# Performance work log

Hardware: AMD Instinct MI355X
Metric: run time of the kernel (lower is better)

Reference implementation:

```python
import jax, jax.numpy as jnp
import numpy as np

D_MODEL = 1024
N_EXPERTS = 8
TOP_K = 2
D_HIDDEN = 4 * D_MODEL


def setup_inputs() -> dict:
    key = jax.random.key(0)
    ks = jax.random.split(key, 6)
    x = jax.random.normal(ks[0], (4, 2048, D_MODEL), dtype=jnp.float32)
    gate_w = jax.random.normal(ks[1], (N_EXPERTS, D_MODEL), dtype=jnp.float32) * 0.02
    w1 = jax.random.normal(ks[2], (N_EXPERTS, D_MODEL, D_HIDDEN), dtype=jnp.float32) * 0.02
    b1 = jnp.zeros((N_EXPERTS, D_HIDDEN), dtype=jnp.float32)
    w2 = jax.random.normal(ks[3], (N_EXPERTS, D_HIDDEN, D_MODEL), dtype=jnp.float32) * 0.02
    b2 = jnp.zeros((N_EXPERTS, D_MODEL), dtype=jnp.float32)
    return {"x": x, "gate_w": gate_w, "w1": w1, "b1": b1, "w2": w2, "b2": b2}


def reference(x, gate_w, w1, b1, w2, b2):
    B, S, D = x.shape
    xf = x.reshape(-1, D)                               # [T, D]
    logits = xf @ gate_w.T                              # [T, E]
    top_vals, top_idx = jax.lax.top_k(logits, TOP_K)    # [T, K]
    rw = jax.nn.softmax(top_vals.astype(jnp.float32), axis=-1).astype(x.dtype)  # [T, K]
    out = jnp.zeros_like(xf)
    for i in range(N_EXPERTS):
        # combined routing weight for expert i per token (0 if not selected)
        cw = jnp.sum(jnp.where(top_idx == i, rw, jnp.zeros_like(rw)), axis=-1)  # [T]
        h = jax.nn.relu(xf @ w1[i] + b1[i])             # [T, 4D]
        y = h @ w2[i] + b2[i]                           # [T, D]
        out = out + y * cw[:, None]
    return out.reshape(B, S, D)
```

## Files before the change

### kernel.cpp

```cpp
#include <hip/hip_runtime.h>
#include <stdint.h>

#define D_MODEL   1024
#define N_EXPERTS 8
#define D_HIDDEN  4096
#define T_TOKENS  8192
#define N_SLOTS   (T_TOKENS * 2)

typedef __bf16 bf16x8 __attribute__((ext_vector_type(8)));
typedef float  f32x4  __attribute__((ext_vector_type(4)));
typedef unsigned short ushort8 __attribute__((ext_vector_type(8)));

__device__ __forceinline__ unsigned short f2bf(float f) {
    unsigned int u = __float_as_uint(f);
    u += 0x7fffu + ((u >> 16) & 1u);
    return (unsigned short)(u >> 16);
}
__device__ __forceinline__ float bf2f(unsigned short v) {
    return __uint_as_float((unsigned int)v << 16);
}

__device__ __forceinline__ void gl_lds16(const void* g, void* l) {
    __builtin_amdgcn_global_load_lds(
        (const __attribute__((address_space(1))) unsigned int*)g,
        (__attribute__((address_space(3))) unsigned int*)l, 16, 0, 0);
}

__global__ __launch_bounds__(256) void gate_kernel(
    const float* __restrict__ x, const float* __restrict__ gw,
    unsigned short* __restrict__ xb,
    int* __restrict__ route_pack, float* __restrict__ route_w,
    int* __restrict__ cnt)
{
    __shared__ float gws[N_EXPERTS * D_MODEL];
    __shared__ int hist[N_EXPERTS];
    int tid = threadIdx.x;
    for (int i = tid * 4; i < N_EXPERTS * D_MODEL; i += 256 * 4)
        *(float4*)&gws[i] = *(const float4*)&gw[i];
    if (tid < N_EXPERTS) hist[tid] = 0;
    __syncthreads();

    int wave = tid >> 6, lane = tid & 63;
    for (int tt = 0; tt < 4; tt++) {
        int t = blockIdx.x * 16 + wave * 4 + tt;
        const float* xr = x + (size_t)t * D_MODEL;

        float acc[N_EXPERTS];
        for (int e = 0; e < N_EXPERTS; e++) acc[e] = 0.f;
        for (int i = 0; i < 4; i++) {
            float4 xv = *(const float4*)&xr[lane * 4 + i * 256];
            ushort4 o;
            o.x = f2bf(xv.x); o.y = f2bf(xv.y); o.z = f2bf(xv.z); o.w = f2bf(xv.w);
            *(ushort4*)&xb[(size_t)t * D_MODEL + lane * 4 + i * 256] = o;
            for (int e = 0; e < N_EXPERTS; e++) {
                float4 gv = *(const float4*)&gws[e * D_MODEL + lane * 4 + i * 256];
                acc[e] += xv.x * gv.x + xv.y * gv.y + xv.z * gv.z + xv.w * gv.w;
            }
        }
        for (int e = 0; e < N_EXPERTS; e++)
            for (int off = 32; off >= 1; off >>= 1)
                acc[e] += __shfl_xor(acc[e], off, 64);

        if (lane == 0) {
            int e0 = 0; float v0 = acc[0];
            for (int e = 1; e < N_EXPERTS; e++) if (acc[e] > v0) { v0 = acc[e]; e0 = e; }
            int e1 = (e0 == 0) ? 1 : 0; float v1 = acc[e1];
            for (int e = 0; e < N_EXPERTS; e++)
                if (e != e0 && acc[e] > v1) { v1 = acc[e]; e1 = e; }
            float w0 = 1.f / (1.f + __expf(v1 - v0));
            route_pack[t] = e0 | (e1 << 8);
            route_w[2 * t]     = w0;
            route_w[2 * t + 1] = 1.f - w0;
            atomicAdd(&hist[e0], 1);
            atomicAdd(&hist[e1], 1);
        }
    }
    __syncthreads();
    if (tid < N_EXPERTS) atomicAdd(&cnt[tid], hist[tid]);
}

__global__ void offsets_kernel(const int* __restrict__ cnt,
                               int* __restrict__ off, int* __restrict__ cnt2)
{
    if (threadIdx.x == 0) {
        int a = 0;
        for (int e = 0; e < N_EXPERTS; e++) { off[e] = a; a += cnt[e]; cnt2[e] = 0; }
        off[N_EXPERTS] = a;
    }
}

__global__ __launch_bounds__(64) void scatter_kernel(
    const int* __restrict__ route_pack, const int* __restrict__ off,
    int* __restrict__ cnt2, int* __restrict__ tok_id, int* __restrict__ inv)
{
    int lane = threadIdx.x;
    int t = blockIdx.x * 64 + lane;
    int p  = route_pack[t];
    int e0 = p & 0xff, e1 = (p >> 8) & 0xff;

    unsigned long long m0[N_EXPERTS], m1[N_EXPERTS];
    for (int e = 0; e < N_EXPERTS; e++) {
        m0[e] = __ballot(e0 == e);
        m1[e] = __ballot(e1 == e);
    }
    int mybase = 0;
    if (lane < N_EXPERTS)
        mybase = atomicAdd(&cnt2[lane], __popcll(m0[lane]) + __popcll(m1[lane]));

    unsigned long long lt = (1ull << lane) - 1ull;
    int b0 = __shfl(mybase, e0);
    int s0 = off[e0] + b0 + (int)__popcll(m0[e0] & lt);
    int b1 = __shfl(mybase, e1);
    int s1 = off[e1] + b1 + (int)__popcll(m0[e1]) + (int)__popcll(m1[e1] & lt);

    tok_id[s0] = t;
    tok_id[s1] = t;
    inv[2 * t]     = s0;
    inv[2 * t + 1] = s1;
}

template <int R, int C>
__global__ __launch_bounds__(256) void transpose_convert_kernel(
    const float* __restrict__ src, unsigned short* __restrict__ dst)
{
    __shared__ float tile[64 * 68];
    int e = blockIdx.z;
    const float* s = src + (size_t)e * R * C;
    unsigned short* d = dst + (size_t)e * R * C;
    int r0 = blockIdx.y * 64, c0 = blockIdx.x * 64;
    int t = threadIdx.x;
    {
        int r = t >> 4, c4 = (t & 15) * 4;
        for (int p = 0; p < 4; p++, r += 16)
            *(float4*)&tile[r * 68 + c4] = *(const float4*)&s[(size_t)(r0 + r) * C + c0 + c4];
    }
    __syncthreads();
    {
        int c = t >> 2, rblk = (t & 3) * 8;
        for (int q = 0; q < 2; q++) {
            int rr = q * 32 + rblk;
            ushort8 o;
            for (int j = 0; j < 8; j++) o[j] = f2bf(tile[(rr + j) * 68 + c]);
            *(ushort8*)&d[(size_t)(c0 + c) * R + r0 + rr] = o;
        }
    }
}

template<int KDIM, int NC, bool RELU, bool USE_TOK>
__global__ __launch_bounds__(512, 2) void moe_gemm_kernel(
    const unsigned short* __restrict__ Ag, const unsigned short* __restrict__ Bw,
    const float* __restrict__ bias, const int* __restrict__ tok_id,
    const int* __restrict__ off, unsigned short* __restrict__ Cout)
{
    constexpr int NT   = KDIM / 64;
    constexpr int NTN  = NC / 256;
    constexpr int NWG  = (N_SLOTS / 256) * NTN;
    constexpr int ASH  = 256 * 64;
    constexpr int BUFS = 2 * ASH;
    __shared__ unsigned short smem[2 * BUFS];

    int wg = blockIdx.x;
    int sz = (wg & 7) * (NWG / 8) + (wg >> 3);
    int bx = sz / NTN;
    int n0 = (sz % NTN) * 256;
    int m0 = bx * 256;

    int tid = threadIdx.x, wave = tid >> 6, lane = tid & 63;
    int wm = wave >> 2, wn = wave & 3;
    int lr = lane >> 3, lc = lane & 7;
    int lcs = lc ^ lr;
    int row16 = lane & 15, qk = lane >> 4;
    int sx = row16 & 7;

    const unsigned short* gA[4];
    const unsigned short* gB[4];
    int ldsA[4], ldsB[4];
#pragma unroll
    for (int c = 0; c < 4; c++) {
        int rowt = wave * 32 + c * 8 + lr;
        int grow;
        if constexpr (USE_TOK) grow = tok_id[m0 + rowt]; else grow = m0 + rowt;
        gA[c] = Ag + (size_t)grow * KDIM + lcs * 8;
        ldsA[c] = (wave * 32 + c * 8) * 64;
        ldsB[c] = ASH + (wave * 32 + c * 8) * 64;
    }

    auto stage = [&](int b, int kt) {
        unsigned short* base = smem + b * BUFS;
#pragma unroll
        for (int c = 0; c < 4; c++) gl_lds16(gA[c] + kt * 64, base + ldsA[c]);
#pragma unroll
        for (int c = 0; c < 4; c++) gl_lds16(gB[c] + kt * 64, base + ldsB[c]);
    };

    for (int e = 0; e < N_EXPERTS; e++) {
        int lo = off[e], hi = off[e + 1];
        if (lo < m0) lo = m0;
        if (hi > m0 + 256) hi = m0 + 256;
        if (lo >= hi) continue;

#pragma unroll
        for (int c = 0; c < 4; c++)
            gB[c] = Bw + ((size_t)e * NC + n0 + wave * 32 + c * 8 + lr) * KDIM + lcs * 8;

        f32x4 acc[8][4];
        const f32x4 zero = {0.f, 0.f, 0.f, 0.f};
#pragma unroll
        for (int i = 0; i < 8; i++)
#pragma unroll
            for (int j = 0; j < 4; j++) acc[i][j] = zero;

        __syncthreads();
        stage(0, 0);
        asm volatile("s_waitcnt vmcnt(0)" ::: "memory");
        __builtin_amdgcn_s_barrier();

        int cur = 0;
        for (int t = 0; t < NT; t++) {
            if (t + 1 < NT) stage(cur ^ 1, t + 1);
            const unsigned short* Ab = smem + cur * BUFS;
            const unsigned short* Bb = Ab + ASH;
            __builtin_amdgcn_s_setprio(1);
#pragma unroll
            for (int ks = 0; ks < 2; ks++) {
                bf16x8 af[8], bq[4];
#pragma unroll
                for (int i = 0; i < 8; i++) {
                    int rr = wm * 128 + i * 16 + row16;
                    af[i] = *(const bf16x8*)&Ab[rr * 64 + (((ks * 4 + qk) ^ sx) * 8)];
                }
#pragma unroll
                for (int j = 0; j < 4; j++) {
                    int br = wn * 64 + j * 16 + row16;
                    bq[j] = *(const bf16x8*)&Bb[br * 64 + (((ks * 4 + qk) ^ sx) * 8)];
                }
#pragma unroll
                for (int i = 0; i < 8; i++)
#pragma unroll
                    for (int j = 0; j < 4; j++)
                        acc[i][j] = __builtin_amdgcn_mfma_f32_16x16x32_bf16(af[i], bq[j], acc[i][j], 0, 0, 0);
            }
            __builtin_amdgcn_s_setprio(0);
            asm volatile("s_waitcnt vmcnt(0)" ::: "memory");
            __builtin_amdgcn_s_barrier();
            cur ^= 1;
        }

        unsigned short* stg = smem;
        int quad = lane >> 4, c16 = lane & 15;
        for (int p = 0; p < 2; p++) {
            if (p) __syncthreads();
            if (wm == p) {
#pragma unroll
                for (int j = 0; j < 4; j++) {
                    int n = n0 + wn * 64 + j * 16 + c16;
                    float bv = bias[e * NC + n];
#pragma unroll
                    for (int i = 0; i < 8; i++)
#pragma unroll
                        for (int r = 0; r < 4; r++) {
                            float v = acc[i][j][r] + bv;
                            if (RELU) v = v > 0.f ? v : 0.f;
                            stg[(i * 16 + quad * 4 + r) * 264 + wn * 64 + j * 16 + c16] = f2bf(v);
                        }
                }
            }
            __syncthreads();
            int srow = tid >> 5, chunk = (tid & 31) * 8;
#pragma unroll
            for (int s8 = 0; s8 < 8; s8++) {
                int rr = srow + s8 * 16;
                int slot = m0 + p * 128 + rr;
                if (slot >= lo && slot < hi)
                    *(ushort8*)&Cout[(size_t)slot * NC + n0 + chunk] =
                        *(const ushort8*)&stg[rr * 264 + chunk];
            }
        }
    }
}

__global__ __launch_bounds__(256) void combine_kernel(
    const unsigned short* __restrict__ y, const int* __restrict__ inv,
    const float* __restrict__ rw, float* __restrict__ out)
{
    int wave = threadIdx.x >> 6, lane = threadIdx.x & 63;
    int t = blockIdx.x * 4 + wave;
    int s0 = inv[2 * t], s1 = inv[2 * t + 1];
    float w0 = rw[2 * t], w1 = rw[2 * t + 1];
    const unsigned short* y0 = y + (size_t)s0 * D_MODEL;
    const unsigned short* y1 = y + (size_t)s1 * D_MODEL;
    float* orow = out + (size_t)t * D_MODEL;
    int c = lane * 16;
    for (int hh = 0; hh < 2; hh++) {
        ushort8 a = *(const ushort8*)&y0[c + hh * 8];
        ushort8 b = *(const ushort8*)&y1[c + hh * 8];
        float4 o0, o1;
        o0.x = w0 * bf2f(a[0]) + w1 * bf2f(b[0]);
        o0.y = w0 * bf2f(a[1]) + w1 * bf2f(b[1]);
        o0.z = w0 * bf2f(a[2]) + w1 * bf2f(b[2]);
        o0.w = w0 * bf2f(a[3]) + w1 * bf2f(b[3]);
        o1.x = w0 * bf2f(a[4]) + w1 * bf2f(b[4]);
        o1.y = w0 * bf2f(a[5]) + w1 * bf2f(b[5]);
        o1.z = w0 * bf2f(a[6]) + w1 * bf2f(b[6]);
        o1.w = w0 * bf2f(a[7]) + w1 * bf2f(b[7]);
        *(float4*)&orow[c + hh * 8]     = o0;
        *(float4*)&orow[c + hh * 8 + 4] = o1;
    }
}

extern "C" void kernel_launch(void* const* d_in, const int* in_sizes, int n_in,
                              void* d_out, int out_size, void* d_ws, size_t ws_size,
                              hipStream_t stream)
{
    const float* x      = (const float*)d_in[0];
    const float* gate_w = (const float*)d_in[1];
    const float* w1     = (const float*)d_in[2];
    const float* b1     = (const float*)d_in[3];
    const float* w2     = (const float*)d_in[4];
    const float* b2     = (const float*)d_in[5];
    float* out = (float*)d_out;

    char* ws = (char*)d_ws;
    size_t o = 0;
    auto alloc = [&](size_t bytes) { void* p = ws + o; o += (bytes + 255) & ~(size_t)255; return p; };
    int*   cnt        = (int*)alloc(32);
    int*   cnt2       = (int*)alloc(32);
    int*   off        = (int*)alloc(64);
    int*   route_pack = (int*)alloc((size_t)T_TOKENS * 4);
    float* route_w    = (float*)alloc((size_t)T_TOKENS * 8);
    int*   tok_id     = (int*)alloc((size_t)N_SLOTS * 4);
    int*   inv        = (int*)alloc((size_t)T_TOKENS * 8);
    unsigned short* xb  = (unsigned short*)alloc((size_t)T_TOKENS * D_MODEL * 2);
    unsigned short* w1t = (unsigned short*)alloc((size_t)N_EXPERTS * D_MODEL * D_HIDDEN * 2);
    unsigned short* w2t = (unsigned short*)alloc((size_t)N_EXPERTS * D_MODEL * D_HIDDEN * 2);
    unsigned short* h   = (unsigned short*)alloc((size_t)N_SLOTS * D_HIDDEN * 2);
    unsigned short* y   = w1t;

    hipMemsetAsync(cnt, 0, 32, stream);

    gate_kernel<<<T_TOKENS / 16, 256, 0, stream>>>(x, gate_w, xb, route_pack, route_w, cnt);
    offsets_kernel<<<1, 64, 0, stream>>>(cnt, off, cnt2);
    scatter_kernel<<<T_TOKENS / 64, 64, 0, stream>>>(route_pack, off, cnt2, tok_id, inv);
    transpose_convert_kernel<D_MODEL, D_HIDDEN>
        <<<dim3(D_HIDDEN / 64, D_MODEL / 64, N_EXPERTS), dim3(256), 0, stream>>>(w1, w1t);
    transpose_convert_kernel<D_HIDDEN, D_MODEL>
        <<<dim3(D_MODEL / 64, D_HIDDEN / 64, N_EXPERTS), dim3(256), 0, stream>>>(w2, w2t);
    moe_gemm_kernel<D_MODEL, D_HIDDEN, true, true>
        <<<dim3((N_SLOTS / 256) * (D_HIDDEN / 256)), dim3(512), 0, stream>>>(xb, w1t, b1, tok_id, off, h);
    moe_gemm_kernel<D_HIDDEN, D_MODEL, false, false>
        <<<dim3((N_SLOTS / 256) * (D_MODEL / 256)), dim3(512), 0, stream>>>(h, w2t, b2, tok_id, off, y);
    combine_kernel<<<T_TOKENS / 4, 256, 0, stream>>>(y, inv, route_w, out);
}
```

Before: 761.1 us.

## Interleave quarter-tile global-to-LDS loads with MFMA phases in expert GEMM

Restructures the expert GEMM main loop into eight sub-phases per two K-tiles. Each phase computes one quarter of the accumulator tile and issues one quarter-tile global-to-LDS stage, using partial vmcnt waits instead of draining all loads each iteration. The goal is to overlap memory traffic with MFMA work and avoid full pipeline stalls, at the cost of more barriers and tricky buffer-hazard ordering.

```diff
diff --git a/kernel.cpp b/kernel.cpp
--- a/kernel.cpp
+++ b/kernel.cpp
@@ -172,26 +172,62 @@
     int row16 = lane & 15, qk = lane >> 4;
     int sx = row16 & 7;
 
-    const unsigned short* gA[4];
-    const unsigned short* gB[4];
-    int ldsA[4], ldsB[4];
-#pragma unroll
-    for (int c = 0; c < 4; c++) {
-        int rowt = wave * 32 + c * 8 + lr;
-        int grow;
-        if constexpr (USE_TOK) grow = tok_id[m0 + rowt]; else grow = m0 + rowt;
-        gA[c] = Ag + (size_t)grow * KDIM + lcs * 8;
-        ldsA[c] = (wave * 32 + c * 8) * 64;
-        ldsB[c] = ASH + (wave * 32 + c * 8) * 64;
-    }
-
-    auto stage = [&](int b, int kt) {
-        unsigned short* base = smem + b * BUFS;
-#pragma unroll
-        for (int c = 0; c < 4; c++) gl_lds16(gA[c] + kt * 64, base + ldsA[c]);
-#pragma unroll
-        for (int c = 0; c < 4; c++) gl_lds16(gB[c] + kt * 64, base + ldsB[c]);
+    const unsigned short* gA[2][2];
+    const unsigned short* gB[2][2];
+    int lbA[2][2], lbB[2][2];
+    int rowA[2][2], rowB[2][2];
+#pragma unroll
+    for (int hh = 0; hh < 2; hh++)
+#pragma unroll
+        for (int c = 0; c < 2; c++) {
+            int q = wave * 16 + c * 8;
+            int ra = (q & 63) + ((q >> 6) << 7) + hh * 64;
+            int rb = (q & 31) + ((q >> 5) << 6) + hh * 32;
+            rowA[hh][c] = ra; rowB[hh][c] = rb;
+            lbA[hh][c] = ra * 64;
+            lbB[hh][c] = ASH + rb * 64;
+            int grow;
+            if constexpr (USE_TOK) grow = tok_id[m0 + ra + lr]; else grow = m0 + ra + lr;
+            gA[hh][c] = Ag + (size_t)grow * KDIM + lcs * 8;
+        }
+
+    auto stA = [&](int b, int hh, int kt) {
+        gl_lds16(gA[hh][0] + kt * 64, smem + b * BUFS + lbA[hh][0]);
+        gl_lds16(gA[hh][1] + kt * 64, smem + b * BUFS + lbA[hh][1]);
     };
+    auto stB = [&](int b, int nn, int kt) {
+        gl_lds16(gB[nn][0] + kt * 64, smem + b * BUFS + lbB[nn][0]);
+        gl_lds16(gB[nn][1] + kt * 64, smem + b * BUFS + lbB[nn][1]);
+    };
+
+#define PHASE(BB, HH, NN, STAGE, VM)                                              \
+    do {                                                                          \
+        const unsigned short* Ab_ = smem + (BB) * BUFS;                           \
+        const unsigned short* Bb_ = Ab_ + ASH;                                    \
+        bf16x8 af[4][2], bq[2][2];                                                \
+        _Pragma("unroll") for (int ii = 0; ii < 4; ii++)                          \
+        _Pragma("unroll") for (int ks = 0; ks < 2; ks++) {                        \
+            int rr = wm * 128 + (HH) * 64 + ii * 16 + row16;                      \
+            af[ii][ks] = *(const bf16x8*)&Ab_[rr * 64 + (((ks * 4 + qk) ^ sx) * 8)]; } \
+        _Pragma("unroll") for (int j = 0; j < 2; j++)                             \
+        _Pragma("unroll") for (int ks = 0; ks < 2; ks++) {                        \
+            int br = wn * 64 + (NN) * 32 + j * 16 + row16;                        \
+            bq[j][ks] = *(const bf16x8*)&Bb_[br * 64 + (((ks * 4 + qk) ^ sx) * 8)]; } \
+        STAGE;                                                                    \
+        __builtin_amdgcn_s_barrier();                                             \
+        __builtin_amdgcn_s_setprio(1);                                            \
+        _Pragma("unroll") for (int ks = 0; ks < 2; ks++)                          \
+        _Pragma("unroll") for (int ii = 0; ii < 4; ii++)                          \
+        _Pragma("unroll") for (int j = 0; j < 2; j++)                             \
+            acc[(HH) * 4 + ii][(NN) * 2 + j] = __builtin_amdgcn_mfma_f32_16x16x32_bf16( \
+                af[ii][ks], bq[j][ks], acc[(HH) * 4 + ii][(NN) * 2 + j], 0, 0, 0);\
+        __builtin_amdgcn_s_setprio(0);                                            \
+        if (VM) asm volatile("s_waitcnt vmcnt(4)" ::: "memory");                  \
+        __builtin_amdgcn_s_barrier();                                             \
+    } while (0)
+
+    f32x4 acc[8][4];
+    const f32x4 zero = {0.f, 0.f, 0.f, 0.f};
 
     for (int e = 0; e < N_EXPERTS; e++) {
         int lo = off[e], hi = off[e + 1];
@@ -200,51 +236,38 @@
         if (lo >= hi) continue;
 
 #pragma unroll
-        for (int c = 0; c < 4; c++)
-            gB[c] = Bw + ((size_t)e * NC + n0 + wave * 32 + c * 8 + lr) * KDIM + lcs * 8;
-
-        f32x4 acc[8][4];
-        const f32x4 zero = {0.f, 0.f, 0.f, 0.f};
+        for (int nn = 0; nn < 2; nn++)
+#pragma unroll
+            for (int c = 0; c < 2; c++)
+                gB[nn][c] = Bw + ((size_t)e * NC + n0 + rowB[nn][c] + lr) * KDIM + lcs * 8;
+
 #pragma unroll
         for (int i = 0; i < 8; i++)
 #pragma unroll
             for (int j = 0; j < 4; j++) acc[i][j] = zero;
 
         __syncthreads();
-        stage(0, 0);
-        asm volatile("s_waitcnt vmcnt(0)" ::: "memory");
+        stA(0, 0, 0); stB(0, 0, 0); stA(0, 1, 0); stB(0, 1, 0);
+        stA(1, 0, 1); stB(1, 0, 1);
+        asm volatile("s_waitcnt vmcnt(4)" ::: "memory");
         __builtin_amdgcn_s_barrier();
 
-        int cur = 0;
-        for (int t = 0; t < NT; t++) {
-            if (t + 1 < NT) stage(cur ^ 1, t + 1);
-            const unsigned short* Ab = smem + cur * BUFS;
-            const unsigned short* Bb = Ab + ASH;
-            __builtin_amdgcn_s_setprio(1);
-#pragma unroll
-            for (int ks = 0; ks < 2; ks++) {
-                bf16x8 af[8], bq[4];
-#pragma unroll
-                for (int i = 0; i < 8; i++) {
-                    int rr = wm * 128 + i * 16 + row16;
-                    af[i] = *(const bf16x8*)&Ab[rr * 64 + (((ks * 4 + qk) ^ sx) * 8)];
-                }
-#pragma unroll
-                for (int j = 0; j < 4; j++) {
-                    int br = wn * 64 + j * 16 + row16;
-                    bq[j] = *(const bf16x8*)&Bb[br * 64 + (((ks * 4 + qk) ^ sx) * 8)];
-                }
-#pragma unroll
-                for (int i = 0; i < 8; i++)
-#pragma unroll
-                    for (int j = 0; j < 4; j++)
-                        acc[i][j] = __builtin_amdgcn_mfma_f32_16x16x32_bf16(af[i], bq[j], acc[i][j], 0, 0, 0);
-            }
-            __builtin_amdgcn_s_setprio(0);
-            asm volatile("s_waitcnt vmcnt(0)" ::: "memory");
-            __builtin_amdgcn_s_barrier();
-            cur ^= 1;
-        }
+        for (int it = 0; it < NT / 2; it++) {
+            int V  = 2 * it + 1;
+            int U2 = (2 * it + 2 < NT) ? 2 * it + 2 : NT - 1;
+            int V2 = (2 * it + 3 < NT) ? 2 * it + 3 : NT - 1;
+            PHASE(0, 0, 0, stA(1, 1, V),  false);
+            PHASE(0, 0, 1, stB(1, 1, V),  false);
+            PHASE(0, 1, 0, stA(0, 0, U2), false);
+            PHASE(0, 1, 1, stB(0, 0, U2), true);
+            PHASE(1, 0, 0, stA(0, 1, U2), false);
+            PHASE(1, 0, 1, stB(0, 1, U2), false);
+            PHASE(1, 1, 0, stA(1, 0, V2), false);
+            PHASE(1, 1, 1, stB(1, 0, V2), true);
+        }
+
+        asm volatile("s_waitcnt vmcnt(0) lgkmcnt(0)" ::: "memory");
+        __syncthreads();
 
         unsigned short* stg = smem;
         int quad = lane >> 4, c16 = lane & 15;
@@ -277,6 +300,7 @@
             }
         }
     }
+#undef PHASE
 }
 
 __global__ __launch_bounds__(256) void combine_kernel(
```

New measurement: 832.0 us. 9.3% more time.
